# Performance work log

Hardware: AMD Instinct MI355X
Metric: run time of the kernel (lower is better)

Reference implementation:

```python
import jax, jax.numpy as jnp
import numpy as np

FEATURE_SIZE = 40960
FIRST_HIDDEN = 512
HALF = FIRST_HIDDEN // 2  # 256, per-perspective width
SECOND_HIDDEN = 32
BATCH = 4096


def setup_inputs() -> dict:
    key = jax.random.key(0)
    ks = jax.random.split(key, 10)
    inp = {
        "white_features": jax.random.uniform(ks[0], (BATCH, FEATURE_SIZE), dtype=jnp.float32),
        "black_features": jax.random.uniform(ks[1], (BATCH, FEATURE_SIZE), dtype=jnp.float32),
        # input_layer1 and input_layer2 share weight_float/bias_float -> single param
        "w_in": jax.random.normal(ks[2], (HALF, FEATURE_SIZE), dtype=jnp.float32) * 0.1,
        "b_in": jnp.zeros((HALF,), dtype=jnp.float32),
        "w_h1": jax.random.normal(ks[3], (SECOND_HIDDEN, FIRST_HIDDEN), dtype=jnp.float32) * 0.1,
        "b_h1": jnp.zeros((SECOND_HIDDEN,), dtype=jnp.float32),
        "w_h2": jax.random.normal(ks[4], (SECOND_HIDDEN, SECOND_HIDDEN), dtype=jnp.float32) * 0.1,
        "b_h2": jnp.zeros((SECOND_HIDDEN,), dtype=jnp.float32),
        "w_out": jax.random.normal(ks[5], (1, SECOND_HIDDEN), dtype=jnp.float32) * 0.1,
        "b_out": jnp.zeros((1,), dtype=jnp.float32),
    }
    return inp


def _clipped_relu(x):
    return jnp.clip(x, 0.0, 1.0)


def reference(white_features, black_features, w_in, b_in, w_h1, b_h1, w_h2, b_h2, w_out, b_out):
    # Perspective feature transform (shared weights), training-mode float path
    out1 = white_features @ w_in.T + b_in  # [B, 256]
    out2 = black_features @ w_in.T + b_in  # [B, 256]
    x = _clipped_relu(jnp.concatenate([out1, out2], axis=1))  # [B, 512]
    x = _clipped_relu(x @ w_h1.T + b_h1)  # [B, 32]
    x = _clipped_relu(x @ w_h2.T + b_h2)  # [B, 32]
    return x @ w_out.T + b_out  # [B, 1]
```

## Files before the change

### kernel.cpp

```cpp
#include <hip/hip_runtime.h>
#include <hip/hip_fp16.h>


#define FEAT 40960
#define PSTRIDE (8192ull * 256ull)
#define KSPLIT 8
#define KCHUNK (FEAT / KSPLIT)
#define NSTEPS (KCHUNK / 32)

using floatx4 = __attribute__((ext_vector_type(4))) float;
using half8   = __attribute__((ext_vector_type(8))) _Float16;
using half4   = __attribute__((ext_vector_type(4))) _Float16;

__device__ __forceinline__ void lds_barrier() {
    asm volatile("s_waitcnt lgkmcnt(0)" ::: "memory");
    __builtin_amdgcn_s_barrier();
}

template <typename PT>
__global__ __launch_bounds__(512, 4) void nnue_gemm8(
    const float* __restrict__ white, const float* __restrict__ black,
    const float* __restrict__ w_in, PT* __restrict__ P)
{
    __shared__ __align__(16) _Float16 As[2][128 * 32];
    __shared__ __align__(16) _Float16 Ws[2][256 * 32];

    const int tid  = threadIdx.x;
    const int lane = tid & 63;
    const int wave = tid >> 6;
    const int wm   = wave >> 2;
    const int wn   = wave & 3;

    const int mb = blockIdx.x & 63;
    const int ks = blockIdx.x >> 6;

    const float* Abase = (mb < 32)
        ? (white + (size_t)mb * 128 * FEAT)
        : (black + (size_t)(mb - 32) * 128 * FEAT);
    const int k0 = ks * KCHUNK;

    const int c4    = tid & 7;
    const int row0  = tid >> 3;
    const int swz_w = ((row0 >> 1) & 3) << 4;
    const int woff  = (c4 * 8) ^ swz_w;

    const int frow  = lane & 15;
    const int fhi   = lane >> 4;
    const int swz_r = ((frow >> 1) & 3) << 4;
    const int kb    = (fhi * 16) ^ swz_r;

    floatx4 acc[4][4];
    const floatx4 zero = {0.f, 0.f, 0.f, 0.f};
#pragma unroll
    for (int m = 0; m < 4; ++m)
#pragma unroll
        for (int n = 0; n < 4; ++n) acc[m][n] = zero;

    floatx4 ra[2], rw[4];

    auto issue = [&](int kglob) {
#pragma unroll
        for (int i = 0; i < 2; ++i)
            ra[i] = *reinterpret_cast<const floatx4*>(
                Abase + (size_t)(row0 + 64 * i) * FEAT + kglob + c4 * 4);
#pragma unroll
        for (int i = 0; i < 4; ++i)
            rw[i] = *reinterpret_cast<const floatx4*>(
                w_in + (size_t)(row0 + 64 * i) * FEAT + kglob + c4 * 4);
    };

    auto cvtStore = [&](int buf) {
#pragma unroll
        for (int i = 0; i < 2; ++i) {
            half4 h;
#pragma unroll
            for (int j = 0; j < 4; ++j) h[j] = (_Float16)ra[i][j];
            *reinterpret_cast<half4*>(
                reinterpret_cast<char*>(&As[buf][0]) + (row0 + 64 * i) * 64 + woff) = h;
        }
#pragma unroll
        for (int i = 0; i < 4; ++i) {
            half4 h;
#pragma unroll
            for (int j = 0; j < 4; ++j) h[j] = (_Float16)rw[i][j];
            *reinterpret_cast<half4*>(
                reinterpret_cast<char*>(&Ws[buf][0]) + (row0 + 64 * i) * 64 + woff) = h;
        }
    };

    auto mfmaStep = [&](int buf) {
        half8 bf[4];
#pragma unroll
        for (int n = 0; n < 4; ++n) {
            const int r = wn * 64 + n * 16 + frow;
            bf[n] = *reinterpret_cast<const half8*>(
                reinterpret_cast<const char*>(&Ws[buf][0]) + r * 64 + kb);
        }
#pragma unroll
        for (int m = 0; m < 4; ++m) {
            const int r = wm * 64 + m * 16 + frow;
            half8 af = *reinterpret_cast<const half8*>(
                reinterpret_cast<const char*>(&As[buf][0]) + r * 64 + kb);
#pragma unroll
            for (int n = 0; n < 4; ++n)
                acc[m][n] = __builtin_amdgcn_mfma_f32_16x16x32_f16(af, bf[n], acc[m][n], 0, 0, 0);
        }
    };

    issue(k0);
    cvtStore(0);
    issue(k0 + 32);
    lds_barrier();

    for (int t = 0; t < NSTEPS; ++t) {
        mfmaStep(t & 1);
        if (t + 1 < NSTEPS) {
            cvtStore((t + 1) & 1);
            if (t + 2 < NSTEPS) issue(k0 + (t + 2) * 32);
        }
        lds_barrier();
    }

    PT* Pb = P + (size_t)ks * PSTRIDE + (size_t)mb * 128 * 256;
#pragma unroll
    for (int m = 0; m < 4; ++m)
#pragma unroll
        for (int n = 0; n < 4; ++n)
#pragma unroll
            for (int r = 0; r < 4; ++r) {
                const int row = wm * 64 + m * 16 + fhi * 4 + r;
                const int col = wn * 64 + n * 16 + frow;
                Pb[(size_t)row * 256 + col] = (PT)acc[m][n][r];
            }
}

template <typename PT>
__global__ __launch_bounds__(256) void nnue_tail8(
    const PT* __restrict__ P,
    const float* __restrict__ b_in,
    const float* __restrict__ w_h1, const float* __restrict__ b_h1,
    const float* __restrict__ w_h2, const float* __restrict__ b_h2,
    const float* __restrict__ w_out, const float* __restrict__ b_out,
    float* __restrict__ out)
{
    __shared__ float xs[32][512];
    __shared__ float w1[32][513];
    __shared__ float w2[32][33];
    __shared__ float h1[32][33];
    __shared__ float h2[32][33];
    __shared__ float wo[32];

    const int tid = threadIdx.x;
    const int b0  = blockIdx.x * 32;

    for (int i = tid; i < 32 * 512; i += 256) w1[i >> 9][i & 511] = w_h1[i];
    for (int i = tid; i < 32 * 32; i += 256)  w2[i >> 5][i & 31]  = w_h2[i];
    if (tid < 32) wo[tid] = w_out[tid];

    for (int i = tid; i < 32 * 512; i += 256) {
        const int r = i >> 9, c = i & 511;
        const int persp = c >> 8, n = c & 255;
        const size_t prow = (size_t)(b0 + r) + (persp ? 4096u : 0u);
        float v = 0.f;
#pragma unroll
        for (int s = 0; s < KSPLIT; ++s)
            v += (float)P[(size_t)s * PSTRIDE + prow * 256 + n];
        v += b_in[n];
        xs[r][c] = fminf(fmaxf(v, 0.f), 1.f);
    }
    __syncthreads();

    for (int p = tid; p < 32 * 32; p += 256) {
        const int o = p & 31, r = p >> 5;
        float a = b_h1[o];
        for (int j = 0; j < 512; ++j) a += xs[r][j] * w1[o][j];
        h1[r][o] = fminf(fmaxf(a, 0.f), 1.f);
    }
    __syncthreads();

    for (int p = tid; p < 32 * 32; p += 256) {
        const int o = p & 31, r = p >> 5;
        float a = b_h2[o];
        for (int j = 0; j < 32; ++j) a += h1[r][j] * w2[o][j];
        h2[r][o] = fminf(fmaxf(a, 0.f), 1.f);
    }
    __syncthreads();

    if (tid < 32) {
        float a = b_out[0];
        for (int j = 0; j < 32; ++j) a += h2[tid][j] * wo[j];
        out[b0 + tid] = a;
    }
}

__global__ __launch_bounds__(256) void nnue_naive(
    const float* __restrict__ white, const float* __restrict__ black,
    const float* __restrict__ w_in, const float* __restrict__ b_in,
    const float* __restrict__ w_h1, const float* __restrict__ b_h1,
    const float* __restrict__ w_h2, const float* __restrict__ b_h2,
    const float* __restrict__ w_out, const float* __restrict__ b_out,
    float* __restrict__ out)
{
    __shared__ float feat[4096];
    __shared__ float xs[512];
    __shared__ float h1s[32];
    __shared__ float h2s[32];
    const int b = blockIdx.x, tid = threadIdx.x;
    float acc0 = 0.f, acc1 = 0.f;
    for (int c = 0; c < FEAT; c += 2048) {
        for (int i = tid; i < 2048; i += 256) {
            feat[i]        = white[(size_t)b * FEAT + c + i];
            feat[2048 + i] = black[(size_t)b * FEAT + c + i];
        }
        __syncthreads();
        const float* wr = w_in + (size_t)tid * FEAT + c;
        for (int k = 0; k < 2048; ++k) {
            const float w = wr[k];
            acc0 += feat[k] * w;
            acc1 += feat[2048 + k] * w;
        }
        __syncthreads();
    }
    xs[tid]       = fminf(fmaxf(acc0 + b_in[tid], 0.f), 1.f);
    xs[256 + tid] = fminf(fmaxf(acc1 + b_in[tid], 0.f), 1.f);
    __syncthreads();
    if (tid < 32) {
        float a = b_h1[tid];
        for (int j = 0; j < 512; ++j) a += xs[j] * w_h1[tid * 512 + j];
        h1s[tid] = fminf(fmaxf(a, 0.f), 1.f);
    }
    __syncthreads();
    if (tid < 32) {
        float a = b_h2[tid];
        for (int j = 0; j < 32; ++j) a += h1s[j] * w_h2[tid * 32 + j];
        h2s[tid] = fminf(fmaxf(a, 0.f), 1.f);
    }
    __syncthreads();
    if (tid == 0) {
        float a = b_out[0];
        for (int j = 0; j < 32; ++j) a += h2s[j] * w_out[j];
        out[b] = a;
    }
}

extern "C" void kernel_launch(void* const* d_in, const int* in_sizes, int n_in,
                              void* d_out, int out_size, void* d_ws, size_t ws_size,
                              hipStream_t stream)
{
    const float* white = (const float*)d_in[0];
    const float* black = (const float*)d_in[1];
    const float* w_in  = (const float*)d_in[2];
    const float* b_in  = (const float*)d_in[3];
    const float* w_h1  = (const float*)d_in[4];
    const float* b_h1  = (const float*)d_in[5];
    const float* w_h2  = (const float*)d_in[6];
    const float* b_h2  = (const float*)d_in[7];
    const float* w_out = (const float*)d_in[8];
    const float* b_out = (const float*)d_in[9];
    float* out = (float*)d_out;

    const size_t f32Need = KSPLIT * PSTRIDE * sizeof(float);
    const size_t f16Need = KSPLIT * PSTRIDE * sizeof(_Float16);

    if (ws_size >= f32Need) {
        float* P = (float*)d_ws;
        nnue_gemm8<float><<<dim3(64 * KSPLIT), 512, 0, stream>>>(white, black, w_in, P);
        nnue_tail8<float><<<dim3(128), 256, 0, stream>>>(P, b_in, w_h1, b_h1,
                                                         w_h2, b_h2, w_out, b_out, out);
    } else if (ws_size >= f16Need) {
        _Float16* P = (_Float16*)d_ws;
        nnue_gemm8<_Float16><<<dim3(64 * KSPLIT), 512, 0, stream>>>(white, black, w_in, P);
        nnue_tail8<_Float16><<<dim3(128), 256, 0, stream>>>(P, b_in, w_h1, b_h1,
                                                            w_h2, b_h2, w_out, b_out, out);
    } else {
        nnue_naive<<<4096, 256, 0, stream>>>(white, black, w_in, b_in, w_h1, b_h1,
                                             w_h2, b_h2, w_out, b_out, out);
    }
}
```

Measured before the change: 420.3 us.

## Pre-convert weights to swizzled fp16 tiles and stream them via direct-to-LDS loads

Adds a prep kernel that converts w_in to fp16 once per call and lays it out in pre-swizzled 16KB tiles in the workspace. The new GEMM kernel loads those tiles with global_load_lds straight into a triple-buffered LDS ring, and double-buffers the activation loads in registers with explicit vmcnt waits. Block indexing is also reordered so the k-split index varies fastest. The goal is to halve weight read traffic, drop the per-block weight conversion, and get deeper prefetch, at the cost of an extra kernel launch, more LDS, and a larger workspace requirement.

```diff
diff --git a/kernel.cpp b/kernel.cpp
--- a/kernel.cpp
+++ b/kernel.cpp
@@ -7,6 +7,8 @@
 #define KSPLIT 8
 #define KCHUNK (FEAT / KSPLIT)
 #define NSTEPS (KCHUNK / 32)
+#define WTILE_BYTES 16384
+#define WWS_BYTES (1280ull * WTILE_BYTES)
 
 using floatx4 = __attribute__((ext_vector_type(4))) float;
 using half8   = __attribute__((ext_vector_type(8))) _Float16;
@@ -15,15 +17,38 @@
 __device__ __forceinline__ void lds_barrier() {
     asm volatile("s_waitcnt lgkmcnt(0)" ::: "memory");
     __builtin_amdgcn_s_barrier();
+    __builtin_amdgcn_sched_barrier(0);
+}
+
+__global__ __launch_bounds__(256) void nnue_wprep(
+    const float* __restrict__ w_in, _Float16* __restrict__ Wws)
+{
+    const int bid = blockIdx.x;
+    const int T   = (bid & 7) * NSTEPS + (bid >> 3);
+    char* base = (char*)Wws + (size_t)T * WTILE_BYTES;
+    const int tid = threadIdx.x;
+    const int kg0 = T * 32;
+#pragma unroll
+    for (int i = 0; i < 4; ++i) {
+        const int G = tid + i * 256;
+        const int r = G >> 2, g = G & 3;
+        const float* src = w_in + (size_t)r * FEAT + kg0 + g * 8;
+        floatx4 v0 = *reinterpret_cast<const floatx4*>(src);
+        floatx4 v1 = *reinterpret_cast<const floatx4*>(src + 4);
+        half8 h;
+#pragma unroll
+        for (int j = 0; j < 4; ++j) { h[j] = (_Float16)v0[j]; h[4 + j] = (_Float16)v1[j]; }
+        *reinterpret_cast<half8*>(base + r * 64 + ((g ^ ((r >> 1) & 3)) << 4)) = h;
+    }
 }
 
 template <typename PT>
-__global__ __launch_bounds__(512, 4) void nnue_gemm8(
+__global__ __launch_bounds__(512, 4) void nnue_gemm_v7(
     const float* __restrict__ white, const float* __restrict__ black,
-    const float* __restrict__ w_in, PT* __restrict__ P)
+    const _Float16* __restrict__ Wws, PT* __restrict__ P)
 {
     __shared__ __align__(16) _Float16 As[2][128 * 32];
-    __shared__ __align__(16) _Float16 Ws[2][256 * 32];
+    __shared__ __align__(16) _Float16 Ws[3][256 * 32];
 
     const int tid  = threadIdx.x;
     const int lane = tid & 63;
@@ -31,8 +56,8 @@
     const int wm   = wave >> 2;
     const int wn   = wave & 3;
 
-    const int mb = blockIdx.x & 63;
-    const int ks = blockIdx.x >> 6;
+    const int ks = blockIdx.x & 7;
+    const int mb = blockIdx.x >> 3;
 
     const float* Abase = (mb < 32)
         ? (white + (size_t)mb * 128 * FEAT)
@@ -41,13 +66,158 @@
 
     const int c4    = tid & 7;
     const int row0  = tid >> 3;
+    const int woff  = (c4 * 8) ^ (((row0 >> 1) & 3) << 4);
+
+    const int frow  = lane & 15;
+    const int fhi   = lane >> 4;
+    const int kb    = (fhi * 16) ^ (((frow >> 1) & 3) << 4);
+
+    const char* wsrc0 = (const char*)Wws + (size_t)(ks * NSTEPS) * WTILE_BYTES
+                        + wave * 2048 + lane * 16;
+
+    floatx4 acc[4][4];
+    const floatx4 zero = {0.f, 0.f, 0.f, 0.f};
+#pragma unroll
+    for (int m = 0; m < 4; ++m)
+#pragma unroll
+        for (int n = 0; n < 4; ++n) acc[m][n] = zero;
+
+    floatx4 ra0[2], ra1[2];
+
+    auto issueA = [&](int kglob, floatx4 (&ra)[2]) {
+#pragma unroll
+        for (int i = 0; i < 2; ++i)
+            ra[i] = *reinterpret_cast<const floatx4*>(
+                Abase + (size_t)(row0 + 64 * i) * FEAT + kglob + c4 * 4);
+    };
+
+    auto issueW = [&](int t, int wb) {
+        const char* g = wsrc0 + (size_t)t * WTILE_BYTES;
+        char* l = (char*)&Ws[wb][0] + wave * 2048;
+        __builtin_amdgcn_global_load_lds(
+            (const __attribute__((address_space(1))) unsigned int*)g,
+            (__attribute__((address_space(3))) unsigned int*)l, 16, 0, 0);
+        __builtin_amdgcn_global_load_lds(
+            (const __attribute__((address_space(1))) unsigned int*)(g + 1024),
+            (__attribute__((address_space(3))) unsigned int*)(l + 1024), 16, 0, 0);
+    };
+
+    auto cvtStoreA = [&](int ab, floatx4 (&ra)[2]) {
+#pragma unroll
+        for (int i = 0; i < 2; ++i) {
+            half4 h;
+#pragma unroll
+            for (int j = 0; j < 4; ++j) h[j] = (_Float16)ra[i][j];
+            *reinterpret_cast<half4*>(
+                reinterpret_cast<char*>(&As[ab][0]) + (row0 + 64 * i) * 64 + woff) = h;
+        }
+    };
+
+    auto mfmaStep = [&](int ab, int wb) {
+        half8 bf[4];
+#pragma unroll
+        for (int n = 0; n < 4; ++n) {
+            const int r = wn * 64 + n * 16 + frow;
+            bf[n] = *reinterpret_cast<const half8*>(
+                reinterpret_cast<const char*>(&Ws[wb][0]) + r * 64 + kb);
+        }
+#pragma unroll
+        for (int m = 0; m < 4; ++m) {
+            const int r = wm * 64 + m * 16 + frow;
+            half8 af = *reinterpret_cast<const half8*>(
+                reinterpret_cast<const char*>(&As[ab][0]) + r * 64 + kb);
+#pragma unroll
+            for (int n = 0; n < 4; ++n)
+                acc[m][n] = __builtin_amdgcn_mfma_f32_16x16x32_f16(af, bf[n], acc[m][n], 0, 0, 0);
+        }
+    };
+
+    auto stepf = [&](int t, int abR, int abW, int wbR, int wbW, floatx4 (&ra)[2]) {
+        issueW(t + 2, wbW);
+        __builtin_amdgcn_sched_barrier(0);
+        mfmaStep(abR, wbR);
+        cvtStoreA(abW, ra);
+        issueA(k0 + (t + 3) * 32, ra);
+        asm volatile("s_waitcnt vmcnt(6) lgkmcnt(0)" ::: "memory");
+        __builtin_amdgcn_s_barrier();
+        __builtin_amdgcn_sched_barrier(0);
+    };
+
+    issueW(0, 0);
+    issueW(1, 1);
+    __builtin_amdgcn_sched_barrier(0);
+    issueA(k0, ra0);
+    issueA(k0 + 32, ra1);
+    cvtStoreA(0, ra0);
+    issueA(k0 + 64, ra0);
+    lds_barrier();
+
+    for (int t = 0; t < 156; t += 6) {
+        stepf(t + 0, 0, 1, 0, 2, ra1);
+        stepf(t + 1, 1, 0, 1, 0, ra0);
+        stepf(t + 2, 0, 1, 2, 1, ra1);
+        stepf(t + 3, 1, 0, 0, 2, ra0);
+        stepf(t + 4, 0, 1, 1, 0, ra1);
+        stepf(t + 5, 1, 0, 2, 1, ra0);
+    }
+    stepf(156, 0, 1, 0, 2, ra1);
+
+    issueW(159, 0);
+    __builtin_amdgcn_sched_barrier(0);
+    mfmaStep(1, 1);
+    cvtStoreA(0, ra0);
+    asm volatile("s_waitcnt vmcnt(4) lgkmcnt(0)" ::: "memory");
+    __builtin_amdgcn_s_barrier();
+    __builtin_amdgcn_sched_barrier(0);
+    mfmaStep(0, 2);
+    cvtStoreA(1, ra1);
+    asm volatile("s_waitcnt vmcnt(0) lgkmcnt(0)" ::: "memory");
+    __builtin_amdgcn_s_barrier();
+    __builtin_amdgcn_sched_barrier(0);
+    mfmaStep(1, 0);
+
+    PT* Pb = P + (size_t)ks * PSTRIDE + (size_t)mb * 128 * 256;
+#pragma unroll
+    for (int m = 0; m < 4; ++m)
+#pragma unroll
+        for (int n = 0; n < 4; ++n)
+#pragma unroll
+            for (int r = 0; r < 4; ++r) {
+                const int row = wm * 64 + m * 16 + fhi * 4 + r;
+                const int col = wn * 64 + n * 16 + frow;
+                Pb[(size_t)row * 256 + col] = (PT)acc[m][n][r];
+            }
+}
+
+template <typename PT>
+__global__ __launch_bounds__(512, 4) void nnue_gemm8(
+    const float* __restrict__ white, const float* __restrict__ black,
+    const float* __restrict__ w_in, PT* __restrict__ P)
+{
+    __shared__ __align__(16) _Float16 As[2][128 * 32];
+    __shared__ __align__(16) _Float16 Ws[2][256 * 32];
+
+    const int tid  = threadIdx.x;
+    const int lane = tid & 63;
+    const int wave = tid >> 6;
+    const int wm   = wave >> 2;
+    const int wn   = wave & 3;
+
+    const int mb = blockIdx.x & 63;
+    const int ks = blockIdx.x >> 6;
+
+    const float* Abase = (mb < 32)
+        ? (white + (size_t)mb * 128 * FEAT)
+        : (black + (size_t)(mb - 32) * 128 * FEAT);
+    const int k0 = ks * KCHUNK;
+
+    const int c4    = tid & 7;
+    const int row0  = tid >> 3;
     const int swz_w = ((row0 >> 1) & 3) << 4;
     const int woff  = (c4 * 8) ^ swz_w;
-
     const int frow  = lane & 15;
     const int fhi   = lane >> 4;
-    const int swz_r = ((frow >> 1) & 3) << 4;
-    const int kb    = (fhi * 16) ^ swz_r;
+    const int kb    = (fhi * 16) ^ (((frow >> 1) & 3) << 4);
 
     floatx4 acc[4][4];
     const floatx4 zero = {0.f, 0.f, 0.f, 0.f};
@@ -259,17 +429,31 @@
     const float* b_out = (const float*)d_in[9];
     float* out = (float*)d_out;
 
-    const size_t f32Need = KSPLIT * PSTRIDE * sizeof(float);
-    const size_t f16Need = KSPLIT * PSTRIDE * sizeof(_Float16);
-
-    if (ws_size >= f32Need) {
+    const size_t pF32 = KSPLIT * PSTRIDE * sizeof(float);
+    const size_t pF16 = KSPLIT * PSTRIDE * sizeof(_Float16);
+
+    if (ws_size >= pF32 + WWS_BYTES) {
         float* P = (float*)d_ws;
-        nnue_gemm8<float><<<dim3(64 * KSPLIT), 512, 0, stream>>>(white, black, w_in, P);
+        _Float16* Wws = (_Float16*)((char*)d_ws + pF32);
+        nnue_wprep<<<dim3(1280), 256, 0, stream>>>(w_in, Wws);
+        nnue_gemm_v7<float><<<dim3(512), 512, 0, stream>>>(white, black, Wws, P);
         nnue_tail8<float><<<dim3(128), 256, 0, stream>>>(P, b_in, w_h1, b_h1,
                                                          w_h2, b_h2, w_out, b_out, out);
-    } else if (ws_size >= f16Need) {
+    } else if (ws_size >= pF16 + WWS_BYTES) {
         _Float16* P = (_Float16*)d_ws;
-        nnue_gemm8<_Float16><<<dim3(64 * KSPLIT), 512, 0, stream>>>(white, black, w_in, P);
+        _Float16* Wws = (_Float16*)((char*)d_ws + pF16);
+        nnue_wprep<<<dim3(1280), 256, 0, stream>>>(w_in, Wws);
+        nnue_gemm_v7<_Float16><<<dim3(512), 512, 0, stream>>>(white, black, Wws, P);
+        nnue_tail8<_Float16><<<dim3(128), 256, 0, stream>>>(P, b_in, w_h1, b_h1,
+                                                            w_h2, b_h2, w_out, b_out, out);
+    } else if (ws_size >= pF32) {
+        float* P = (float*)d_ws;
+        nnue_gemm8<float><<<dim3(512), 512, 0, stream>>>(white, black, w_in, P);
+        nnue_tail8<float><<<dim3(128), 256, 0, stream>>>(P, b_in, w_h1, b_h1,
+                                                         w_h2, b_h2, w_out, b_out, out);
+    } else if (ws_size >= pF16) {
+        _Float16* P = (_Float16*)d_ws;
+        nnue_gemm8<_Float16><<<dim3(512), 512, 0, stream>>>(white, black, w_in, P);
         nnue_tail8<_Float16><<<dim3(128), 256, 0, stream>>>(P, b_in, w_h1, b_h1,
                                                             w_h2, b_h2, w_out, b_out, out);
     } else {
```

Result: faster. 382.4 us (-9.0%).

## Pre-convert weights to swizzled fp16 chunks and stream them via direct-to-LDS loads

Applied to the files above, without the earlier changes.

Adds a prep kernel that converts w_in to fp16 once per call, stored in swizzled 64-column chunks in workspace. The GEMM then loads these chunks directly into LDS with global_load_lds, triple-buffered, instead of loading fp32 weights and converting them inside every block. The K-split drops from 8 to 4, the block grows to 1024 threads with a 128x256 tile and 128-wide K steps, and software pipelining uses explicit vmcnt waits. The aim is to cut redundant weight conversion and traffic and the partial-sum traffic, at the cost of an extra kernel, more workspace, and lower occupancy from larger LDS use.

```diff
diff --git a/kernel.cpp b/kernel.cpp
--- a/kernel.cpp
+++ b/kernel.cpp
@@ -4,26 +4,50 @@
 
 #define FEAT 40960
 #define PSTRIDE (8192ull * 256ull)
-#define KSPLIT 8
-#define KCHUNK (FEAT / KSPLIT)
-#define NSTEPS (KCHUNK / 32)
+#define KS4 4
+#define KCHUNK4 (FEAT / KS4)
+#define NSUPER 80
+#define WCHUNK_BYTES 32768
+#define NWCHUNK 640
+#define WWS_BYTES ((size_t)NWCHUNK * WCHUNK_BYTES)
 
 using floatx4 = __attribute__((ext_vector_type(4))) float;
 using half8   = __attribute__((ext_vector_type(8))) _Float16;
 using half4   = __attribute__((ext_vector_type(4))) _Float16;
 
-__device__ __forceinline__ void lds_barrier() {
-    asm volatile("s_waitcnt lgkmcnt(0)" ::: "memory");
-    __builtin_amdgcn_s_barrier();
+__device__ __forceinline__ void gload16(const char* g, char* l) {
+    __builtin_amdgcn_global_load_lds(
+        (const __attribute__((address_space(1))) unsigned int*)g,
+        (__attribute__((address_space(3))) unsigned int*)l, 16, 0, 0);
+}
+
+__global__ __launch_bounds__(256) void nnue_wprep64(
+    const float* __restrict__ w_in, _Float16* __restrict__ Wws)
+{
+    const int C   = blockIdx.x;
+    char* base = (char*)Wws + (size_t)C * WCHUNK_BYTES;
+    const int tid = threadIdx.x;
+#pragma unroll
+    for (int i = 0; i < 8; ++i) {
+        const int S = tid + i * 256;
+        const int r = S >> 3, g = S & 7;
+        const float* src = w_in + (size_t)r * FEAT + C * 64 + g * 8;
+        floatx4 v0 = *reinterpret_cast<const floatx4*>(src);
+        floatx4 v1 = *reinterpret_cast<const floatx4*>(src + 4);
+        half8 h;
+#pragma unroll
+        for (int j = 0; j < 4; ++j) { h[j] = (_Float16)v0[j]; h[4 + j] = (_Float16)v1[j]; }
+        *reinterpret_cast<half8*>(base + r * 128 + ((g ^ ((r >> 1) & 7)) << 4)) = h;
+    }
 }
 
 template <typename PT>
-__global__ __launch_bounds__(512, 4) void nnue_gemm8(
+__global__ __launch_bounds__(1024, 4) void nnue_gemm_v8(
     const float* __restrict__ white, const float* __restrict__ black,
-    const float* __restrict__ w_in, PT* __restrict__ P)
-{
-    __shared__ __align__(16) _Float16 As[2][128 * 32];
-    __shared__ __align__(16) _Float16 Ws[2][256 * 32];
+    const _Float16* __restrict__ Wws, PT* __restrict__ P)
+{
+    __shared__ __align__(16) _Float16 As[2][128 * 128];
+    __shared__ __align__(16) _Float16 Ws[3][256 * 64];
 
     const int tid  = threadIdx.x;
     const int lane = tid & 63;
@@ -31,112 +55,149 @@
     const int wm   = wave >> 2;
     const int wn   = wave & 3;
 
-    const int mb = blockIdx.x & 63;
-    const int ks = blockIdx.x >> 6;
+    const int ks = blockIdx.x & 3;
+    const int mb = blockIdx.x >> 2;
 
     const float* Abase = (mb < 32)
         ? (white + (size_t)mb * 128 * FEAT)
         : (black + (size_t)(mb - 32) * 128 * FEAT);
-    const int k0 = ks * KCHUNK;
-
-    const int c4    = tid & 7;
-    const int row0  = tid >> 3;
-    const int swz_w = ((row0 >> 1) & 3) << 4;
-    const int woff  = (c4 * 8) ^ swz_w;
-
-    const int frow  = lane & 15;
-    const int fhi   = lane >> 4;
-    const int swz_r = ((frow >> 1) & 3) << 4;
-    const int kb    = (fhi * 16) ^ swz_r;
-
-    floatx4 acc[4][4];
+    const int k0 = ks * KCHUNK4;
+
+    const float* Arow = Abase + (size_t)(tid >> 5) * FEAT + (tid & 31) * 4;
+    const int aoff = (tid >> 5) * 256 + (((tid & 31) * 8) ^ ((wave & 7) << 4));
+
+    const int frow = lane & 15;
+    const int fhi  = lane >> 4;
+    const int swzr = ((frow >> 1) & 7) << 4;
+
+    const char* wsrc0 = (const char*)Wws + (size_t)(ks * 160) * WCHUNK_BYTES
+                        + wave * 2048 + lane * 16;
+
+    floatx4 acc[2][4];
     const floatx4 zero = {0.f, 0.f, 0.f, 0.f};
 #pragma unroll
-    for (int m = 0; m < 4; ++m)
+    for (int m = 0; m < 2; ++m)
 #pragma unroll
         for (int n = 0; n < 4; ++n) acc[m][n] = zero;
 
-    floatx4 ra[2], rw[4];
-
-    auto issue = [&](int kglob) {
-#pragma unroll
-        for (int i = 0; i < 2; ++i)
-            ra[i] = *reinterpret_cast<const floatx4*>(
-                Abase + (size_t)(row0 + 64 * i) * FEAT + kglob + c4 * 4);
-#pragma unroll
-        for (int i = 0; i < 4; ++i)
-            rw[i] = *reinterpret_cast<const floatx4*>(
-                w_in + (size_t)(row0 + 64 * i) * FEAT + kglob + c4 * 4);
+    floatx4 rc0, rc1, rc2, rc3;
+
+    auto issueW = [&](int T, int wb) {
+        const char* g = wsrc0 + (size_t)T * WCHUNK_BYTES;
+        char* l = (char*)&Ws[wb][0] + wave * 2048;
+        gload16(g, l);
+        gload16(g + 1024, l + 1024);
     };
 
-    auto cvtStore = [&](int buf) {
-#pragma unroll
-        for (int i = 0; i < 2; ++i) {
-            half4 h;
-#pragma unroll
-            for (int j = 0; j < 4; ++j) h[j] = (_Float16)ra[i][j];
-            *reinterpret_cast<half4*>(
-                reinterpret_cast<char*>(&As[buf][0]) + (row0 + 64 * i) * 64 + woff) = h;
-        }
-#pragma unroll
-        for (int i = 0; i < 4; ++i) {
-            half4 h;
-#pragma unroll
-            for (int j = 0; j < 4; ++j) h[j] = (_Float16)rw[i][j];
-            *reinterpret_cast<half4*>(
-                reinterpret_cast<char*>(&Ws[buf][0]) + (row0 + 64 * i) * 64 + woff) = h;
+    auto issueA = [&](floatx4& rc, int j, int kg) {
+        rc = *reinterpret_cast<const floatx4*>(Arow + (size_t)j * 32 * FEAT + kg);
+    };
+
+    auto cvtStore = [&](floatx4& rc, int j, int ab) {
+        half4 h;
+#pragma unroll
+        for (int jj = 0; jj < 4; ++jj) h[jj] = (_Float16)rc[jj];
+        *reinterpret_cast<half4*>(
+            reinterpret_cast<char*>(&As[ab][0]) + aoff + j * 8192) = h;
+    };
+
+    auto mfmaSub = [&](int ab, int cLit, int wb) {
+        const char* wbase = (const char*)&Ws[wb][0];
+        const char* abase = (const char*)&As[ab][0];
+#pragma unroll
+        for (int kk = 0; kk < 2; ++kk) {
+            half8 bf[4];
+#pragma unroll
+            for (int n = 0; n < 4; ++n) {
+                const int r = wn * 64 + n * 16 + frow;
+                bf[n] = *reinterpret_cast<const half8*>(
+                    wbase + r * 128 + ((kk * 64 + fhi * 16) ^ swzr));
+            }
+#pragma unroll
+            for (int m = 0; m < 2; ++m) {
+                const int row = wm * 32 + m * 16 + frow;
+                half8 af = *reinterpret_cast<const half8*>(
+                    abase + row * 256 + ((cLit * 128 + kk * 64 + fhi * 16) ^ swzr));
+#pragma unroll
+                for (int n = 0; n < 4; ++n)
+                    acc[m][n] = __builtin_amdgcn_mfma_f32_16x16x32_f16(af, bf[n], acc[m][n], 0, 0, 0);
+            }
         }
     };
 
-    auto mfmaStep = [&](int buf) {
-        half8 bf[4];
-#pragma unroll
-        for (int n = 0; n < 4; ++n) {
-            const int r = wn * 64 + n * 16 + frow;
-            bf[n] = *reinterpret_cast<const half8*>(
-                reinterpret_cast<const char*>(&Ws[buf][0]) + r * 64 + kb);
-        }
-#pragma unroll
-        for (int m = 0; m < 4; ++m) {
-            const int r = wm * 64 + m * 16 + frow;
-            half8 af = *reinterpret_cast<const half8*>(
-                reinterpret_cast<const char*>(&As[buf][0]) + r * 64 + kb);
-#pragma unroll
-            for (int n = 0; n < 4; ++n)
-                acc[m][n] = __builtin_amdgcn_mfma_f32_16x16x32_f16(af, bf[n], acc[m][n], 0, 0, 0);
-        }
-    };
-
-    issue(k0);
-    cvtStore(0);
-    issue(k0 + 32);
-    lds_barrier();
-
-    for (int t = 0; t < NSTEPS; ++t) {
-        mfmaStep(t & 1);
-        if (t + 1 < NSTEPS) {
-            cvtStore((t + 1) & 1);
-            if (t + 2 < NSTEPS) issue(k0 + (t + 2) * 32);
-        }
-        lds_barrier();
-    }
+    issueW(0, 0);
+    issueW(1, 1);
+    __builtin_amdgcn_sched_barrier(0);
+    issueA(rc0, 0, k0); issueA(rc1, 1, k0); issueA(rc2, 2, k0); issueA(rc3, 3, k0);
+    cvtStore(rc0, 0, 0); cvtStore(rc1, 1, 0); cvtStore(rc2, 2, 0); cvtStore(rc3, 3, 0);
+    issueA(rc0, 0, k0 + 128); issueA(rc1, 1, k0 + 128);
+    issueA(rc2, 2, k0 + 128); issueA(rc3, 3, k0 + 128);
+    asm volatile("s_waitcnt lgkmcnt(0)" ::: "memory");
+    __builtin_amdgcn_s_barrier();
+    __builtin_amdgcn_sched_barrier(0);
+
+    int wr0 = 0;
+    for (int s = 0; s < 78; ++s) {
+        const int abR = s & 1;
+        const int abW = abR ^ 1;
+        const int wr1 = (wr0 + 1) % 3;
+        const int wb0 = (wr0 + 2) % 3;
+        const int kg  = k0 + (s + 2) * 128;
+        issueW(2 * s + 2, wb0);
+        __builtin_amdgcn_sched_barrier(0);
+        mfmaSub(abR, 0, wr0);
+        cvtStore(rc0, 0, abW); cvtStore(rc1, 1, abW);
+        issueA(rc0, 0, kg); issueA(rc1, 1, kg);
+        asm volatile("s_waitcnt vmcnt(6) lgkmcnt(0)" ::: "memory");
+        __builtin_amdgcn_s_barrier();
+        __builtin_amdgcn_sched_barrier(0);
+        issueW(2 * s + 3, wr0);
+        __builtin_amdgcn_sched_barrier(0);
+        mfmaSub(abR, 1, wr1);
+        cvtStore(rc2, 2, abW); cvtStore(rc3, 3, abW);
+        issueA(rc2, 2, kg); issueA(rc3, 3, kg);
+        asm volatile("s_waitcnt vmcnt(6) lgkmcnt(0)" ::: "memory");
+        __builtin_amdgcn_s_barrier();
+        __builtin_amdgcn_sched_barrier(0);
+        wr0 = (wr0 + 2) % 3;
+    }
+
+    issueW(158, 2);
+    __builtin_amdgcn_sched_barrier(0);
+    mfmaSub(0, 0, 0);
+    cvtStore(rc0, 0, 1); cvtStore(rc1, 1, 1);
+    asm volatile("s_waitcnt vmcnt(4) lgkmcnt(0)" ::: "memory");
+    __builtin_amdgcn_s_barrier();
+    __builtin_amdgcn_sched_barrier(0);
+    issueW(159, 0);
+    __builtin_amdgcn_sched_barrier(0);
+    mfmaSub(0, 1, 1);
+    cvtStore(rc2, 2, 1); cvtStore(rc3, 3, 1);
+    asm volatile("s_waitcnt vmcnt(2) lgkmcnt(0)" ::: "memory");
+    __builtin_amdgcn_s_barrier();
+    __builtin_amdgcn_sched_barrier(0);
+    mfmaSub(1, 0, 2);
+    asm volatile("s_waitcnt vmcnt(0) lgkmcnt(0)" ::: "memory");
+    __builtin_amdgcn_s_barrier();
+    __builtin_amdgcn_sched_barrier(0);
+    mfmaSub(1, 1, 0);
 
     PT* Pb = P + (size_t)ks * PSTRIDE + (size_t)mb * 128 * 256;
 #pragma unroll
-    for (int m = 0; m < 4; ++m)
+    for (int m = 0; m < 2; ++m)
 #pragma unroll
         for (int n = 0; n < 4; ++n)
 #pragma unroll
             for (int r = 0; r < 4; ++r) {
-                const int row = wm * 64 + m * 16 + fhi * 4 + r;
+                const int row = wm * 32 + m * 16 + fhi * 4 + r;
                 const int col = wn * 64 + n * 16 + frow;
                 Pb[(size_t)row * 256 + col] = (PT)acc[m][n][r];
             }
 }
 
 template <typename PT>
-__global__ __launch_bounds__(256) void nnue_tail8(
-    const PT* __restrict__ P,
+__global__ __launch_bounds__(256) void nnue_tail(
+    const PT* __restrict__ P, int KS,
     const float* __restrict__ b_in,
     const float* __restrict__ w_h1, const float* __restrict__ b_h1,
     const float* __restrict__ w_h2, const float* __restrict__ b_h2,
@@ -162,8 +223,7 @@
         const int persp = c >> 8, n = c & 255;
         const size_t prow = (size_t)(b0 + r) + (persp ? 4096u : 0u);
         float v = 0.f;
-#pragma unroll
-        for (int s = 0; s < KSPLIT; ++s)
+        for (int s = 0; s < KS; ++s)
             v += (float)P[(size_t)s * PSTRIDE + prow * 256 + n];
         v += b_in[n];
         xs[r][c] = fminf(fmaxf(v, 0.f), 1.f);
@@ -259,19 +319,23 @@
     const float* b_out = (const float*)d_in[9];
     float* out = (float*)d_out;
 
-    const size_t f32Need = KSPLIT * PSTRIDE * sizeof(float);
-    const size_t f16Need = KSPLIT * PSTRIDE * sizeof(_Float16);
-
-    if (ws_size >= f32Need) {
+    const size_t pF32 = KS4 * PSTRIDE * sizeof(float);
+    const size_t pF16 = KS4 * PSTRIDE * sizeof(_Float16);
+
+    if (ws_size >= pF32 + WWS_BYTES) {
         float* P = (float*)d_ws;
-        nnue_gemm8<float><<<dim3(64 * KSPLIT), 512, 0, stream>>>(white, black, w_in, P);
-        nnue_tail8<float><<<dim3(128), 256, 0, stream>>>(P, b_in, w_h1, b_h1,
-                                                         w_h2, b_h2, w_out, b_out, out);
-    } else if (ws_size >= f16Need) {
+        _Float16* Wws = (_Float16*)((char*)d_ws + pF32);
+        nnue_wprep64<<<dim3(NWCHUNK), 256, 0, stream>>>(w_in, Wws);
+        nnue_gemm_v8<float><<<dim3(256), 1024, 0, stream>>>(white, black, Wws, P);
+        nnue_tail<float><<<dim3(128), 256, 0, stream>>>(P, KS4, b_in, w_h1, b_h1,
+                                                        w_h2, b_h2, w_out, b_out, out);
+    } else if (ws_size >= pF16 + WWS_BYTES) {
         _Float16* P = (_Float16*)d_ws;
-        nnue_gemm8<_Float16><<<dim3(64 * KSPLIT), 512, 0, stream>>>(white, black, w_in, P);
-        nnue_tail8<_Float16><<<dim3(128), 256, 0, stream>>>(P, b_in, w_h1, b_h1,
-                                                            w_h2, b_h2, w_out, b_out, out);
+        _Float16* Wws = (_Float16*)((char*)d_ws + pF16);
+        nnue_wprep64<<<dim3(NWCHUNK), 256, 0, stream>>>(w_in, Wws);
+        nnue_gemm_v8<_Float16><<<dim3(256), 1024, 0, stream>>>(white, black, Wws, P);
+        nnue_tail<_Float16><<<dim3(128), 256, 0, stream>>>(P, KS4, b_in, w_h1, b_h1,
+                                                           w_h2, b_h2, w_out, b_out, out);
     } else {
         nnue_naive<<<4096, 256, 0, stream>>>(white, black, w_in, b_in, w_h1, b_h1,
                                              w_h2, b_h2, w_out, b_out, out);
```

Result: faster. 383.3 us (-8.8%).
